# Kernel tuning notes

Hardware: AMD Instinct MI355X
Metric: run time of the kernel (lower is better)

Reference implementation:

```python
import jax, jax.numpy as jnp
import numpy as np

N_NODES = 100000
N_EDGES = 1600000
HID = 128
EDGE_DIM = 32
GN_EPS = 1e-5


def setup_inputs() -> dict:
    key = jax.random.key(0)
    ks = jax.random.split(key, 8)
    s = 0.05
    return {
        "x": jax.random.normal(ks[0], (N_NODES, HID), jnp.float32),
        "edge_index": jax.random.randint(ks[1], (2, N_EDGES), 0, N_NODES, jnp.int64),
        "edge_attr": jax.random.normal(ks[2], (N_EDGES, EDGE_DIM), jnp.float32),
        "edge_lin_W": jax.random.normal(ks[3], (EDGE_DIM, HID), jnp.float32) * s,
        "edge_lin_b": jnp.zeros((HID,), jnp.float32),
        "mlp_W1": jax.random.normal(ks[4], (HID, HID), jnp.float32) * s,
        "mlp_b1": jnp.zeros((HID,), jnp.float32),
        "mlp_W2": jax.random.normal(ks[5], (HID, HID), jnp.float32) * s,
        "mlp_b2": jnp.zeros((HID,), jnp.float32),
        "gn_weight": jnp.ones((HID,), jnp.float32),
        "gn_bias": jnp.zeros((HID,), jnp.float32),
        "gn_mean_scale": jnp.ones((HID,), jnp.float32),
    }


def reference(x, edge_index, edge_attr, edge_lin_W, edge_lin_b,
              mlp_W1, mlp_b1, mlp_W2, mlp_b2,
              gn_weight, gn_bias, gn_mean_scale):
    src, dst = edge_index[0], edge_index[1]
    # GINEConv message: ReLU(x_j + Lin(edge_attr)), sum-aggregated at dst
    e = edge_attr @ edge_lin_W + edge_lin_b            # [E, HID]
    msg = jax.nn.relu(x[src] + e)                      # [E, HID]
    agg = jax.ops.segment_sum(msg, dst, num_segments=x.shape[0])  # [N, HID]
    # update MLP on (1+eps)*x + agg, eps = 0
    h = agg + x
    h = jax.nn.relu(h @ mlp_W1 + mlp_b1) @ mlp_W2 + mlp_b2
    # GraphNorm with batch=None -> single graph: global node stats
    mean = jnp.mean(h, axis=0, keepdims=True)          # [1, HID]
    sub = h - gn_mean_scale * mean
    var = jnp.mean(sub * sub, axis=0, keepdims=True)
    out = gn_weight * sub / jnp.sqrt(var + GN_EPS) + gn_bias
    # final ReLU; dropout is identity at eval
    return jax.nn.relu(out)
```

## Files before the change

### kernel.cpp

```cpp
#include <hip/hip_runtime.h>
#include <stdint.h>

#define HID 128
#define EDIM 32

typedef __attribute__((ext_vector_type(8))) short bf16x8;
typedef __attribute__((ext_vector_type(4))) float f4_t;

static __device__ __forceinline__ unsigned short f2bf(float f) {
  union { float f; unsigned int u; } v; v.f = f;
  return (unsigned short)((v.u + 0x7fffu + ((v.u >> 16) & 1u)) >> 16);
}

static __device__ __forceinline__ float bf2f(short s) {
  union { unsigned int u; float f; } v;
  v.u = ((unsigned int)(unsigned short)s) << 16;
  return v.f;
}

static __device__ __forceinline__ void atomAddF(float* p, float v) {
#if defined(__gfx950__) || defined(__gfx942__) || defined(__gfx90a__)
  unsafeAtomicAdd(p, v);
#else
  atomicAdd(p, v);
#endif
}

__global__ __launch_bounds__(256) void hist_xperm(const int* __restrict__ ei,
                                                  const float* __restrict__ x,
                                                  unsigned int* __restrict__ counts,
                                                  unsigned short* __restrict__ xPerm,
                                                  int nE, int nNodes, int doPerm) {
  int tid = blockIdx.x * blockDim.x + threadIdx.x;
  const int stride = gridDim.x * blockDim.x;
  for (int i = tid; i < nE; i += stride) atomicAdd(&counts[ei[nE + i]], 1u);
  if (doPerm) {
    const int nCh = nNodes * 16;
    for (int j = tid; j < nCh; j += stride) {
      const int node = j >> 4, g = j & 15;
      const float* xp = x + (size_t)node * HID + g;
      bf16x8 o;
#pragma unroll
      for (int k = 0; k < 8; ++k) o[k] = (short)f2bf(xp[k * 16]);
      *(bf16x8*)(xPerm + (size_t)node * HID + g * 8) = o;
    }
  }
}

__global__ __launch_bounds__(1024) void chunk_sum(const unsigned int* __restrict__ counts,
                                                  unsigned int* __restrict__ chunkSum, int N) {
  __shared__ unsigned int wsum[16];
  const int tid = threadIdx.x;
  const int i = blockIdx.x * 1024 + tid;
  unsigned int v = (i < N) ? counts[i] : 0u;
#pragma unroll
  for (int d = 1; d < 64; d <<= 1) v += (unsigned int)__shfl_xor((int)v, d);
  if ((tid & 63) == 0) wsum[tid >> 6] = v;
  __syncthreads();
  if (tid < 16) {
    unsigned int t = wsum[tid];
#pragma unroll
    for (int d = 1; d < 16; d <<= 1) t += (unsigned int)__shfl_xor((int)t, d);
    if (tid == 0) chunkSum[blockIdx.x] = t;
  }
}

__global__ __launch_bounds__(256) void scan_chunks(const unsigned int* __restrict__ chunkSum,
                                                   unsigned int* __restrict__ chunkOff,
                                                   unsigned int* __restrict__ offsets,
                                                   int nChunks, int N) {
  __shared__ unsigned int wsum[4];
  const int tid = threadIdx.x, lane = tid & 63, w = tid >> 6;
  unsigned int v = (tid < nChunks) ? chunkSum[tid] : 0u;
  unsigned int s = v;
#pragma unroll
  for (int d = 1; d < 64; d <<= 1) {
    unsigned int t = (unsigned int)__shfl_up((int)s, d);
    if (lane >= d) s += t;
  }
  if (lane == 63) wsum[w] = s;
  __syncthreads();
  unsigned int wOff = 0;
  for (int k = 0; k < w; ++k) wOff += wsum[k];
  if (tid < nChunks) chunkOff[tid] = wOff + s - v;
  if (tid == nChunks - 1) offsets[N] = wOff + s;
}

__global__ __launch_bounds__(1024) void scan_local(const unsigned int* __restrict__ counts,
                                                   const unsigned int* __restrict__ chunkOff,
                                                   unsigned int* __restrict__ offsets,
                                                   unsigned int* __restrict__ cursors, int N) {
  __shared__ unsigned int wsum[16];
  const int tid = threadIdx.x, lane = tid & 63, w = tid >> 6;
  const int i = blockIdx.x * 1024 + tid;
  unsigned int v = (i < N) ? counts[i] : 0u;
  unsigned int s = v;
#pragma unroll
  for (int d = 1; d < 64; d <<= 1) {
    unsigned int t = (unsigned int)__shfl_up((int)s, d);
    if (lane >= d) s += t;
  }
  if (lane == 63) wsum[w] = s;
  __syncthreads();
  unsigned int wOff = 0;
  for (int k = 0; k < w; ++k) wOff += wsum[k];
  if (i < N) {
    const unsigned int ex = chunkOff[blockIdx.x] + wOff + (s - v);
    offsets[i] = ex;
    cursors[i] = ex;
  }
}

__global__ __launch_bounds__(256) void scatter_conv(const int* __restrict__ ei,
                                                    const float* __restrict__ ea,
                                                    unsigned int* __restrict__ cursors,
                                                    unsigned int* __restrict__ sortedSrc,
                                                    unsigned short* __restrict__ eaSorted,
                                                    int nE) {
  const int lane = threadIdx.x & 63;
  const int q = lane & 3;
  int t = blockIdx.x * blockDim.x + threadIdx.x;
  const int eStride = (gridDim.x * blockDim.x) >> 2;
  for (int e = t >> 2; e < nE; e += eStride) {
    unsigned int pos = 0;
    if (q == 0) {
      const int d = ei[nE + e];
      pos = atomicAdd(&cursors[d], 1u);
      sortedSrc[pos] = (unsigned int)ei[e];
    }
    pos = (unsigned int)__shfl((int)pos, lane & ~3);
    const f4_t* ap = (const f4_t*)(ea + (size_t)e * EDIM + q * 8);
    f4_t a0 = __builtin_nontemporal_load(ap);
    f4_t a1 = __builtin_nontemporal_load(ap + 1);
    bf16x8 o;
#pragma unroll
    for (int k = 0; k < 4; ++k) { o[k] = (short)f2bf(a0[k]); o[k + 4] = (short)f2bf(a1[k]); }
    *(bf16x8*)(eaSorted + (size_t)pos * EDIM + q * 8) = o;
  }
}

__global__ __launch_bounds__(256) void scatter_min(const int* __restrict__ ei,
                                                   unsigned int* __restrict__ cursors,
                                                   unsigned int* __restrict__ sortedEid,
                                                   unsigned int* __restrict__ sortedSrc,
                                                   int nE) {
  int i = blockIdx.x * blockDim.x + threadIdx.x;
  const int stride = gridDim.x * blockDim.x;
  for (; i < nE; i += stride) {
    const int d = ei[nE + i];
    const unsigned int pos = atomicAdd(&cursors[d], 1u);
    sortedEid[pos] = (unsigned int)i;
    sortedSrc[pos] = (unsigned int)ei[i];
  }
}

__global__ __launch_bounds__(256) void agg_pair(
    const float* __restrict__ x, const unsigned short* __restrict__ xPerm,
    const unsigned short* __restrict__ eaSorted, const unsigned int* __restrict__ sortedSrc,
    const float* __restrict__ W, const float* __restrict__ bias,
    const unsigned int* __restrict__ offsets, float* __restrict__ h,
    int nNodes, int nPairs) {
  const int lane = threadIdx.x & 63;
  const int l15 = lane & 15;
  const int lq  = lane >> 4;

  bf16x8 Wf[8];
  float bv[8];
#pragma unroll
  for (int nt = 0; nt < 8; ++nt) {
#pragma unroll
    for (int j = 0; j < 8; ++j)
      Wf[nt][j] = (short)f2bf(W[(8 * lq + j) * HID + 16 * nt + l15]);
    bv[nt] = bias[16 * nt + l15];
  }

  int waveId = blockIdx.x * 4 + ((int)threadIdx.x >> 6);
  const int nWaves = gridDim.x * 4;

  auto LOADT = [&](unsigned int b, unsigned int end, bf16x8& af, bf16x8* xg) {
    const unsigned int sA = b + (unsigned int)l15;
    if (sA < end)
      af = __builtin_nontemporal_load((const bf16x8*)(eaSorted + (size_t)sA * EDIM + lq * 8));
    else
      af = bf16x8{0, 0, 0, 0, 0, 0, 0, 0};
#pragma unroll
    for (int r = 0; r < 4; ++r) {
      unsigned int sl = b + (unsigned int)(lq * 4 + r);
      unsigned int cl = sl < end ? sl : end - 1;
      const unsigned int src = sortedSrc[cl];
      xg[r] = *(const bf16x8*)(xPerm + (size_t)src * HID + l15 * 8);
    }
  };

  for (int p = waveId; p < nPairs; p += nWaves) {
    const int nA = p * 2;
    const int nB = (nA + 1 < nNodes) ? nA + 1 : nA;
    unsigned int bA = offsets[nA];
    const unsigned int eA = offsets[nA + 1];
    unsigned int bB = offsets[nB];
    const unsigned int eB = offsets[nB + 1];

    float accA[8] = {0, 0, 0, 0, 0, 0, 0, 0};
    float accB[8] = {0, 0, 0, 0, 0, 0, 0, 0};

    while (bA < eA || bB < eB) {
      const bool mA = bA < eA, mB = bB < eB;
      bf16x8 afA, afB, xgA[4], xgB[4];
      if (mA) LOADT(bA, eA, afA, xgA);
      if (mB) LOADT(bB, eB, afB, xgB);

      if (mA) {
        f4_t acc[8];
#pragma unroll
        for (int nt = 0; nt < 8; ++nt) {
          f4_t c; c[0] = bv[nt]; c[1] = bv[nt]; c[2] = bv[nt]; c[3] = bv[nt];
          acc[nt] = __builtin_amdgcn_mfma_f32_16x16x32_bf16(afA, Wf[nt], c, 0, 0, 0);
        }
#pragma unroll
        for (int r = 0; r < 4; ++r) {
          if (bA + (unsigned int)(lq * 4 + r) < eA) {
#pragma unroll
            for (int nt = 0; nt < 8; ++nt)
              accA[nt] += fmaxf(acc[nt][r] + bf2f(xgA[r][nt]), 0.f);
          }
        }
        bA += 16;
      }

      if (mB) {
        f4_t acc[8];
#pragma unroll
        for (int nt = 0; nt < 8; ++nt) {
          f4_t c; c[0] = bv[nt]; c[1] = bv[nt]; c[2] = bv[nt]; c[3] = bv[nt];
          acc[nt] = __builtin_amdgcn_mfma_f32_16x16x32_bf16(afB, Wf[nt], c, 0, 0, 0);
        }
#pragma unroll
        for (int r = 0; r < 4; ++r) {
          if (bB + (unsigned int)(lq * 4 + r) < eB) {
#pragma unroll
            for (int nt = 0; nt < 8; ++nt)
              accB[nt] += fmaxf(acc[nt][r] + bf2f(xgB[r][nt]), 0.f);
          }
        }
        bB += 16;
      }
    }

#pragma unroll
    for (int nt = 0; nt < 8; ++nt) {
      accA[nt] += __shfl_xor(accA[nt], 16);
      accA[nt] += __shfl_xor(accA[nt], 32);
      accB[nt] += __shfl_xor(accB[nt], 16);
      accB[nt] += __shfl_xor(accB[nt], 32);
    }

    const int c0 = 32 * lq + l15;
    const size_t rowA = (size_t)nA * HID;
    const size_t rowB = (size_t)nB * HID;
    h[rowA + c0]      = accA[2 * lq]     + x[rowA + c0];
    h[rowA + c0 + 16] = accA[2 * lq + 1] + x[rowA + c0 + 16];
    h[rowB + c0]      = accB[2 * lq]     + x[rowB + c0];
    h[rowB + c0 + 16] = accB[2 * lq + 1] + x[rowB + c0 + 16];
  }
}

__global__ __launch_bounds__(256) void agg_fb(
    const float* __restrict__ x, const float* __restrict__ ea,
    const float* __restrict__ W, const float* __restrict__ bias,
    const unsigned int* __restrict__ offsets, const unsigned int* __restrict__ sortedEid,
    const unsigned int* __restrict__ sortedSrc, float* __restrict__ h, int nNodes) {
  const int lane = threadIdx.x & 63;
  const int l15 = lane & 15;
  const int lq  = lane >> 4;

  bf16x8 Wf[8];
  float bv[8];
#pragma unroll
  for (int nt = 0; nt < 8; ++nt) {
#pragma unroll
    for (int j = 0; j < 8; ++j)
      Wf[nt][j] = (short)f2bf(W[(8 * lq + j) * HID + 16 * nt + l15]);
    bv[nt] = bias[16 * nt + l15];
  }

  int waveId = blockIdx.x * 4 + ((int)threadIdx.x >> 6);
  const int nWaves = gridDim.x * 4;

  for (int n = waveId; n < nNodes; n += nWaves) {
    const unsigned int beg = offsets[n];
    const unsigned int end = offsets[n + 1];
    float accv[8] = {0, 0, 0, 0, 0, 0, 0, 0};

    for (unsigned int base = beg; base < end; base += 16) {
      bf16x8 af = {0, 0, 0, 0, 0, 0, 0, 0};
      const unsigned int slotA = base + (unsigned int)l15;
      if (slotA < end) {
        const unsigned int eidA = sortedEid[slotA];
        const float* ap = ea + (size_t)eidA * EDIM + 8 * lq;
        f4_t a0 = *(const f4_t*)ap;
        f4_t a1 = *(const f4_t*)(ap + 4);
#pragma unroll
        for (int j = 0; j < 4; ++j) { af[j] = (short)f2bf(a0[j]); af[j + 4] = (short)f2bf(a1[j]); }
      }
      f4_t acc[8];
#pragma unroll
      for (int nt = 0; nt < 8; ++nt) {
        f4_t c; c[0] = bv[nt]; c[1] = bv[nt]; c[2] = bv[nt]; c[3] = bv[nt];
        acc[nt] = __builtin_amdgcn_mfma_f32_16x16x32_bf16(af, Wf[nt], c, 0, 0, 0);
      }
#pragma unroll
      for (int r = 0; r < 4; ++r) {
        const unsigned int slot = base + (unsigned int)(lq * 4 + r);
        if (slot < end) {
          const int s = (int)sortedSrc[slot];
          const float* xp = x + (size_t)s * HID + l15;
#pragma unroll
          for (int nt = 0; nt < 8; ++nt)
            accv[nt] += fmaxf(acc[nt][r] + xp[nt * 16], 0.f);
        }
      }
    }

#pragma unroll
    for (int nt = 0; nt < 8; ++nt) {
      accv[nt] += __shfl_xor(accv[nt], 16);
      accv[nt] += __shfl_xor(accv[nt], 32);
    }
    const int c0 = 32 * lq + l15;
    const size_t rowOff = (size_t)n * HID;
    h[rowOff + c0]      = accv[2 * lq]     + x[rowOff + c0];
    h[rowOff + c0 + 16] = accv[2 * lq + 1] + x[rowOff + c0 + 16];
  }
}

__global__ __launch_bounds__(256) void node_kernel(
    float* __restrict__ h, const float* __restrict__ W1, const float* __restrict__ b1,
    const float* __restrict__ W2, const float* __restrict__ b2,
    float* __restrict__ stats, int nNodes, int nTiles) {
  __shared__ unsigned short sW1[128 * 128];
  __shared__ unsigned short sW2[128 * 128];
  __shared__ unsigned short sH1[4][16 * 128];

  for (int idx = threadIdx.x; idx < 128 * 128; idx += 256) {
    int n = idx & 127, k = idx >> 7;
    int off = n * 128 + ((((k >> 3) ^ (n & 15))) << 3) + (k & 7);
    sW1[off] = f2bf(W1[k * HID + n]);
    sW2[off] = f2bf(W2[k * HID + n]);
  }
  __syncthreads();

  const int lane = threadIdx.x & 63;
  const int l15 = lane & 15, lq = lane >> 4;
  const int wv = threadIdx.x >> 6;
  unsigned short* hb = &sH1[wv][0];

  float b1v[8], b2v[8];
#pragma unroll
  for (int nt = 0; nt < 8; ++nt) { b1v[nt] = b1[nt * 16 + l15]; b2v[nt] = b2[nt * 16 + l15]; }
  float ssum[8] = {0, 0, 0, 0, 0, 0, 0, 0};
  float ssq[8]  = {0, 0, 0, 0, 0, 0, 0, 0};

  int waveId = blockIdx.x * 4 + wv;
  const int nWaves = gridDim.x * 4;

  for (int tile = waveId; tile < nTiles; tile += nWaves) {
    const int r0 = tile << 4;
    int rr = r0 + l15; if (rr >= nNodes) rr = nNodes - 1;
    const float* hp = h + (size_t)rr * HID;

    bf16x8 af[4];
#pragma unroll
    for (int kt = 0; kt < 4; ++kt) {
      const int k0 = kt * 32 + 8 * lq;
      f4_t u0 = *(const f4_t*)(hp + k0);
      f4_t u1 = *(const f4_t*)(hp + k0 + 4);
#pragma unroll
      for (int j = 0; j < 4; ++j) {
        af[kt][j]     = (short)f2bf(u0[j]);
        af[kt][j + 4] = (short)f2bf(u1[j]);
      }
    }

    f4_t acc[8];
#pragma unroll
    for (int nt = 0; nt < 8; ++nt) {
      f4_t c; c[0] = b1v[nt]; c[1] = b1v[nt]; c[2] = b1v[nt]; c[3] = b1v[nt];
#pragma unroll
      for (int kt = 0; kt < 4; ++kt) {
        bf16x8 wf = *(const bf16x8*)&sW1[(nt * 16 + l15) * 128 + ((((kt * 4 + lq) ^ l15)) << 3)];
        c = __builtin_amdgcn_mfma_f32_16x16x32_bf16(af[kt], wf, c, 0, 0, 0);
      }
      acc[nt] = c;
    }

#pragma unroll
    for (int nt = 0; nt < 8; ++nt) {
      const int ghi = 2 * nt + (l15 >> 3);
#pragma unroll
      for (int r = 0; r < 4; ++r) {
        const int row = lq * 4 + r;
        hb[row * 128 + ((ghi ^ (row & 15)) << 3) + (l15 & 7)] = f2bf(fmaxf(acc[nt][r], 0.f));
      }
    }
    asm volatile("s_waitcnt lgkmcnt(0)" ::: "memory");
    __builtin_amdgcn_sched_barrier(0);

    bf16x8 af2[4];
#pragma unroll
    for (int kt = 0; kt < 4; ++kt)
      af2[kt] = *(const bf16x8*)&hb[l15 * 128 + ((((kt * 4 + lq) ^ l15)) << 3)];

    f4_t acc2[8];
#pragma unroll
    for (int nt = 0; nt < 8; ++nt) {
      f4_t c; c[0] = b2v[nt]; c[1] = b2v[nt]; c[2] = b2v[nt]; c[3] = b2v[nt];
#pragma unroll
      for (int kt = 0; kt < 4; ++kt) {
        bf16x8 wf = *(const bf16x8*)&sW2[(nt * 16 + l15) * 128 + ((((kt * 4 + lq) ^ l15)) << 3)];
        c = __builtin_amdgcn_mfma_f32_16x16x32_bf16(af2[kt], wf, c, 0, 0, 0);
      }
      acc2[nt] = c;
    }

#pragma unroll
    for (int nt = 0; nt < 8; ++nt) {
#pragma unroll
      for (int r = 0; r < 4; ++r) {
        const int row = r0 + lq * 4 + r;
        if (row < nNodes) {
          float v = acc2[nt][r];
          h[(size_t)row * HID + nt * 16 + l15] = v;
          ssum[nt] += v; ssq[nt] += v * v;
        }
      }
    }
  }

#pragma unroll
  for (int nt = 0; nt < 8; ++nt) {
    float a = ssum[nt], b = ssq[nt];
    a += __shfl_xor(a, 16); b += __shfl_xor(b, 16);
    a += __shfl_xor(a, 32); b += __shfl_xor(b, 32);
    if (lq == 0) {
      atomAddF(&stats[nt * 16 + l15], a);
      atomAddF(&stats[HID + nt * 16 + l15], b);
    }
  }
}

__global__ void norm_prep(float* __restrict__ stats, const float* __restrict__ gw,
                          const float* __restrict__ gb, const float* __restrict__ gs,
                          int nNodes) {
  int c = threadIdx.x;
  if (c < HID) {
    float invN = 1.f / (float)nNodes;
    float m   = stats[c] * invN;
    float msq = stats[HID + c] * invN;
    float s   = gs[c];
    float var = msq - (2.f * s - s * s) * m * m;
    float A = gw[c] * rsqrtf(var + 1e-5f);
    float B = gb[c] - A * s * m;
    stats[2 * HID + c] = A;
    stats[3 * HID + c] = B;
  }
}

__global__ __launch_bounds__(256) void norm_kernel(const float* __restrict__ stats,
                                                   float* __restrict__ out, int total4) {
  const f4_t* A4 = (const f4_t*)(stats + 2 * HID);
  const f4_t* B4 = (const f4_t*)(stats + 3 * HID);
  int i = blockIdx.x * blockDim.x + threadIdx.x;
  const int stride = gridDim.x * blockDim.x;
  for (; i < total4; i += stride) {
    const int cg = i & 31;
    f4_t h = ((const f4_t*)out)[i];
    f4_t a = A4[cg], b = B4[cg];
    f4_t o;
#pragma unroll
    for (int j = 0; j < 4; ++j) o[j] = fmaxf(fmaf(h[j], a[j], b[j]), 0.f);
    ((f4_t*)out)[i] = o;
  }
}

extern "C" void kernel_launch(void* const* d_in, const int* in_sizes, int n_in,
                              void* d_out, int out_size, void* d_ws, size_t ws_size,
                              hipStream_t stream) {
  const float* x  = (const float*)d_in[0];
  const int*   ei = (const int*)d_in[1];
  const float* ea = (const float*)d_in[2];
  const float* eW = (const float*)d_in[3];
  const float* eb = (const float*)d_in[4];
  const float* W1 = (const float*)d_in[5];
  const float* b1 = (const float*)d_in[6];
  const float* W2 = (const float*)d_in[7];
  const float* b2 = (const float*)d_in[8];
  const float* gw = (const float*)d_in[9];
  const float* gb = (const float*)d_in[10];
  const float* gs = (const float*)d_in[11];
  float* out = (float*)d_out;

  const int nNodes = in_sizes[0] / HID;
  const int nE     = in_sizes[1] / 2;

  char* w = (char*)d_ws;
  const size_t offStats   = 0;
  const size_t offCounts  = 2048;
  const size_t offCursors = offCounts  + (size_t)nNodes * 4;
  const size_t offOffsets = offCursors + (size_t)nNodes * 4;
  const size_t offChunk   = offOffsets + (((size_t)(nNodes + 1) * 4 + 63) & ~63ull);
  const size_t offSS      = (offChunk + 2048 + 63) & ~63ull;
  const size_t offEaS     = offSS + (size_t)nE * 4;
  const size_t offXP      = offEaS + (size_t)nE * EDIM * 2;
  const size_t needFlat   = offXP + (size_t)nNodes * HID * 2;

  float* stats            = (float*)(w + offStats);
  unsigned int* counts    = (unsigned int*)(w + offCounts);
  unsigned int* cursors   = (unsigned int*)(w + offCursors);
  unsigned int* offsets   = (unsigned int*)(w + offOffsets);
  unsigned int* chunkSum  = (unsigned int*)(w + offChunk);
  unsigned int* chunkOff  = (unsigned int*)(w + offChunk + 1024);
  unsigned int* sortedSrc = (unsigned int*)(w + offSS);
  unsigned int* sortedEid = (unsigned int*)(w + offEaS);
  unsigned short* eaSorted= (unsigned short*)(w + offEaS);
  unsigned short* xPerm   = (unsigned short*)(w + offXP);

  const int flatMode = (ws_size >= needFlat) ? 1 : 0;

  hipMemsetAsync(d_ws, 0, offCursors, stream);

  hist_xperm<<<2048, 256, 0, stream>>>(ei, x, counts, xPerm, nE, nNodes, flatMode);

  const int nChunks = (nNodes + 1023) / 1024;
  chunk_sum<<<nChunks, 1024, 0, stream>>>(counts, chunkSum, nNodes);
  scan_chunks<<<1, 256, 0, stream>>>(chunkSum, chunkOff, offsets, nChunks, nNodes);
  scan_local<<<nChunks, 1024, 0, stream>>>(counts, chunkOff, offsets, cursors, nNodes);

  if (flatMode) {
    scatter_conv<<<2048, 256, 0, stream>>>(ei, ea, cursors, sortedSrc, eaSorted, nE);
    const int nPairs = (nNodes + 1) / 2;
    const int blocks = (nPairs + 7) / 8;
    agg_pair<<<blocks, 256, 0, stream>>>(x, xPerm, eaSorted, sortedSrc, eW, eb,
                                         offsets, out, nNodes, nPairs);
  } else {
    scatter_min<<<1024, 256, 0, stream>>>(ei, cursors, sortedEid, sortedSrc, nE);
    agg_fb<<<8192, 256, 0, stream>>>(x, ea, eW, eb, offsets, sortedEid, sortedSrc, out, nNodes);
  }

  const int nTiles = (nNodes + 15) >> 4;
  node_kernel<<<512, 256, 0, stream>>>(out, W1, b1, W2, b2, stats, nNodes, nTiles);

  norm_prep<<<1, 128, 0, stream>>>(stats, gw, gb, gs, nNodes);
  norm_kernel<<<2048, 256, 0, stream>>>(stats, out, nNodes * (HID / 4));
}
```

Before: 419.6 us.

## Aggregate three nodes per wave, prefetch source indices, store h in bf16

The aggregation kernel now handles three destination nodes per wave instead of two, giving more independent gathers in flight. It preloads up to 128 source indices with one coalesced load and hands them out by wave shuffles instead of scalar reads. When workspace allows, the aggregated h is written as bf16 into a separate buffer, so node_kernel reads half the bytes and skips its conversion. The cost is more register pressure from three accumulator sets and a larger workspace requirement.

Measured after the change: 497.0 us. 18.5% more time.

```diff
diff --git a/kernel.cpp b/kernel.cpp
--- a/kernel.cpp
+++ b/kernel.cpp
@@ -154,12 +154,13 @@
   }
 }
 
-__global__ __launch_bounds__(256) void agg_pair(
+template <int BF16H>
+__global__ __launch_bounds__(256) void agg_tri(
     const float* __restrict__ x, const unsigned short* __restrict__ xPerm,
     const unsigned short* __restrict__ eaSorted, const unsigned int* __restrict__ sortedSrc,
     const float* __restrict__ W, const float* __restrict__ bias,
     const unsigned int* __restrict__ offsets, float* __restrict__ h,
-    int nNodes, int nPairs) {
+    unsigned short* __restrict__ hBf, int nNodes, int nGroups) {
   const int lane = threadIdx.x & 63;
   const int l15 = lane & 15;
   const int lq  = lane >> 4;
@@ -177,90 +178,116 @@
   int waveId = blockIdx.x * 4 + ((int)threadIdx.x >> 6);
   const int nWaves = gridDim.x * 4;
 
-  auto LOADT = [&](unsigned int b, unsigned int end, bf16x8& af, bf16x8* xg) {
-    const unsigned int sA = b + (unsigned int)l15;
-    if (sA < end)
-      af = __builtin_nontemporal_load((const bf16x8*)(eaSorted + (size_t)sA * EDIM + lq * 8));
-    else
-      af = bf16x8{0, 0, 0, 0, 0, 0, 0, 0};
-#pragma unroll
-    for (int r = 0; r < 4; ++r) {
-      unsigned int sl = b + (unsigned int)(lq * 4 + r);
-      unsigned int cl = sl < end ? sl : end - 1;
-      const unsigned int src = sortedSrc[cl];
-      xg[r] = *(const bf16x8*)(xPerm + (size_t)src * HID + l15 * 8);
-    }
-  };
-
-  for (int p = waveId; p < nPairs; p += nWaves) {
-    const int nA = p * 2;
-    const int nB = (nA + 1 < nNodes) ? nA + 1 : nA;
-    unsigned int bA = offsets[nA];
-    const unsigned int eA = offsets[nA + 1];
-    unsigned int bB = offsets[nB];
-    const unsigned int eB = offsets[nB + 1];
-
-    float accA[8] = {0, 0, 0, 0, 0, 0, 0, 0};
-    float accB[8] = {0, 0, 0, 0, 0, 0, 0, 0};
-
-    while (bA < eA || bB < eB) {
-      const bool mA = bA < eA, mB = bB < eB;
-      bf16x8 afA, afB, xgA[4], xgB[4];
-      if (mA) LOADT(bA, eA, afA, xgA);
-      if (mB) LOADT(bB, eB, afB, xgB);
-
-      if (mA) {
-        f4_t acc[8];
-#pragma unroll
-        for (int nt = 0; nt < 8; ++nt) {
-          f4_t c; c[0] = bv[nt]; c[1] = bv[nt]; c[2] = bv[nt]; c[3] = bv[nt];
-          acc[nt] = __builtin_amdgcn_mfma_f32_16x16x32_bf16(afA, Wf[nt], c, 0, 0, 0);
+  for (int g = waveId; g < nGroups; g += nWaves) {
+    const int n0 = g * 3;
+    unsigned int beg[3], end[3];
+#pragma unroll
+    for (int m = 0; m < 3; ++m) {
+      const int nm = n0 + m;
+      if (nm < nNodes) { beg[m] = offsets[nm]; end[m] = offsets[nm + 1]; }
+      else { beg[m] = 0; end[m] = 0; }
+    }
+    const unsigned int s0 = beg[0];
+    unsigned int endC = end[2] > end[1] ? end[2] : end[1];
+    endC = endC > end[0] ? endC : end[0];
+
+    unsigned int srcP0 = 0, srcP1 = 0;
+    if (endC > s0) {
+      const unsigned int last = endC - 1;
+      unsigned int i0 = s0 + (unsigned int)lane;
+      unsigned int i1 = i0 + 64;
+      srcP0 = __builtin_nontemporal_load(&sortedSrc[i0 < last ? i0 : last]);
+      srcP1 = __builtin_nontemporal_load(&sortedSrc[i1 < last ? i1 : last]);
+    }
+
+    auto GETSRC = [&](unsigned int slot) -> unsigned int {
+      const int idx = (int)(slot - s0);
+      const unsigned int v0 = (unsigned int)__shfl((int)srcP0, idx & 63);
+      const unsigned int v1 = (unsigned int)__shfl((int)srcP1, idx & 63);
+      unsigned int v = (idx < 64) ? v0 : v1;
+      if (idx >= 128) v = sortedSrc[slot];
+      return v;
+    };
+
+    auto LOADT = [&](unsigned int b, unsigned int e, bf16x8& af, bf16x8* xg) {
+      const unsigned int sA = b + (unsigned int)l15;
+      if (sA < e)
+        af = __builtin_nontemporal_load((const bf16x8*)(eaSorted + (size_t)sA * EDIM + lq * 8));
+      else
+        af = bf16x8{0, 0, 0, 0, 0, 0, 0, 0};
+#pragma unroll
+      for (int r = 0; r < 4; ++r) {
+        unsigned int sl = b + (unsigned int)(lq * 4 + r);
+        unsigned int cl = sl < e ? sl : e - 1;
+        const unsigned int src = GETSRC(cl);
+        xg[r] = *(const bf16x8*)(xPerm + (size_t)src * HID + l15 * 8);
+      }
+    };
+
+    float acc0[8] = {0, 0, 0, 0, 0, 0, 0, 0};
+    float acc1[8] = {0, 0, 0, 0, 0, 0, 0, 0};
+    float acc2[8] = {0, 0, 0, 0, 0, 0, 0, 0};
+    float* accs[3] = {acc0, acc1, acc2};
+    unsigned int cur[3] = {beg[0], beg[1], beg[2]};
+
+    while (cur[0] < end[0] || cur[1] < end[1] || cur[2] < end[2]) {
+      bool mm[3];
+      bf16x8 af[3], xg[3][4];
+#pragma unroll
+      for (int m = 0; m < 3; ++m) {
+        mm[m] = cur[m] < end[m];
+        if (mm[m]) LOADT(cur[m], end[m], af[m], xg[m]);
+      }
+#pragma unroll
+      for (int m = 0; m < 3; ++m) {
+        if (mm[m]) {
+          f4_t acc[8];
+#pragma unroll
+          for (int nt = 0; nt < 8; ++nt) {
+            f4_t c; c[0] = bv[nt]; c[1] = bv[nt]; c[2] = bv[nt]; c[3] = bv[nt];
+            acc[nt] = __builtin_amdgcn_mfma_f32_16x16x32_bf16(af[m], Wf[nt], c, 0, 0, 0);
+          }
+          float* av = accs[m];
+#pragma unroll
+          for (int r = 0; r < 4; ++r) {
+            if (cur[m] + (unsigned int)(lq * 4 + r) < end[m]) {
+#pragma unroll
+              for (int nt = 0; nt < 8; ++nt)
+                av[nt] += fmaxf(acc[nt][r] + bf2f(xg[m][r][nt]), 0.f);
+            }
+          }
+          cur[m] += 16;
         }
-#pragma unroll
-        for (int r = 0; r < 4; ++r) {
-          if (bA + (unsigned int)(lq * 4 + r) < eA) {
-#pragma unroll
-            for (int nt = 0; nt < 8; ++nt)
-              accA[nt] += fmaxf(acc[nt][r] + bf2f(xgA[r][nt]), 0.f);
-          }
+      }
+    }
+
+#pragma unroll
+    for (int m = 0; m < 3; ++m) {
+      float* av = accs[m];
+#pragma unroll
+      for (int nt = 0; nt < 8; ++nt) {
+        av[nt] += __shfl_xor(av[nt], 16);
+        av[nt] += __shfl_xor(av[nt], 32);
+      }
+    }
+
+    const int c0 = 32 * lq + l15;
+#pragma unroll
+    for (int m = 0; m < 3; ++m) {
+      const int nm = n0 + m;
+      if (nm < nNodes) {
+        const size_t row = (size_t)nm * HID;
+        const float v0 = accs[m][2 * lq]     + x[row + c0];
+        const float v1 = accs[m][2 * lq + 1] + x[row + c0 + 16];
+        if (BF16H) {
+          hBf[row + c0]      = f2bf(v0);
+          hBf[row + c0 + 16] = f2bf(v1);
+        } else {
+          h[row + c0]      = v0;
+          h[row + c0 + 16] = v1;
         }
-        bA += 16;
-      }
-
-      if (mB) {
-        f4_t acc[8];
-#pragma unroll
-        for (int nt = 0; nt < 8; ++nt) {
-          f4_t c; c[0] = bv[nt]; c[1] = bv[nt]; c[2] = bv[nt]; c[3] = bv[nt];
-          acc[nt] = __builtin_amdgcn_mfma_f32_16x16x32_bf16(afB, Wf[nt], c, 0, 0, 0);
-        }
-#pragma unroll
-        for (int r = 0; r < 4; ++r) {
-          if (bB + (unsigned int)(lq * 4 + r) < eB) {
-#pragma unroll
-            for (int nt = 0; nt < 8; ++nt)
-              accB[nt] += fmaxf(acc[nt][r] + bf2f(xgB[r][nt]), 0.f);
-          }
-        }
-        bB += 16;
-      }
-    }
-
-#pragma unroll
-    for (int nt = 0; nt < 8; ++nt) {
-      accA[nt] += __shfl_xor(accA[nt], 16);
-      accA[nt] += __shfl_xor(accA[nt], 32);
-      accB[nt] += __shfl_xor(accB[nt], 16);
-      accB[nt] += __shfl_xor(accB[nt], 32);
-    }
-
-    const int c0 = 32 * lq + l15;
-    const size_t rowA = (size_t)nA * HID;
-    const size_t rowB = (size_t)nB * HID;
-    h[rowA + c0]      = accA[2 * lq]     + x[rowA + c0];
-    h[rowA + c0 + 16] = accA[2 * lq + 1] + x[rowA + c0 + 16];
-    h[rowB + c0]      = accB[2 * lq]     + x[rowB + c0];
-    h[rowB + c0 + 16] = accB[2 * lq + 1] + x[rowB + c0 + 16];
+      }
+    }
   }
 }
 
@@ -333,10 +360,12 @@
   }
 }
 
+template <int BF16H>
 __global__ __launch_bounds__(256) void node_kernel(
-    float* __restrict__ h, const float* __restrict__ W1, const float* __restrict__ b1,
+    const float* __restrict__ hF, const unsigned short* __restrict__ hBf,
+    const float* __restrict__ W1, const float* __restrict__ b1,
     const float* __restrict__ W2, const float* __restrict__ b2,
-    float* __restrict__ stats, int nNodes, int nTiles) {
+    float* __restrict__ h2out, float* __restrict__ stats, int nNodes, int nTiles) {
   __shared__ unsigned short sW1[128 * 128];
   __shared__ unsigned short sW2[128 * 128];
   __shared__ unsigned short sH1[4][16 * 128];
@@ -366,18 +395,25 @@
   for (int tile = waveId; tile < nTiles; tile += nWaves) {
     const int r0 = tile << 4;
     int rr = r0 + l15; if (rr >= nNodes) rr = nNodes - 1;
-    const float* hp = h + (size_t)rr * HID;
 
     bf16x8 af[4];
-#pragma unroll
-    for (int kt = 0; kt < 4; ++kt) {
-      const int k0 = kt * 32 + 8 * lq;
-      f4_t u0 = *(const f4_t*)(hp + k0);
-      f4_t u1 = *(const f4_t*)(hp + k0 + 4);
-#pragma unroll
-      for (int j = 0; j < 4; ++j) {
-        af[kt][j]     = (short)f2bf(u0[j]);
-        af[kt][j + 4] = (short)f2bf(u1[j]);
+    if (BF16H) {
+      const unsigned short* hp = hBf + (size_t)rr * HID;
+#pragma unroll
+      for (int kt = 0; kt < 4; ++kt)
+        af[kt] = *(const bf16x8*)(hp + kt * 32 + 8 * lq);
+    } else {
+      const float* hp = hF + (size_t)rr * HID;
+#pragma unroll
+      for (int kt = 0; kt < 4; ++kt) {
+        const int k0 = kt * 32 + 8 * lq;
+        f4_t u0 = *(const f4_t*)(hp + k0);
+        f4_t u1 = *(const f4_t*)(hp + k0 + 4);
+#pragma unroll
+        for (int j = 0; j < 4; ++j) {
+          af[kt][j]     = (short)f2bf(u0[j]);
+          af[kt][j + 4] = (short)f2bf(u1[j]);
+        }
       }
     }
 
@@ -429,7 +465,7 @@
         const int row = r0 + lq * 4 + r;
         if (row < nNodes) {
           float v = acc2[nt][r];
-          h[(size_t)row * HID + nt * 16 + l15] = v;
+          h2out[(size_t)row * HID + nt * 16 + l15] = v;
           ssum[nt] += v; ssq[nt] += v * v;
         }
       }
@@ -512,6 +548,8 @@
   const size_t offEaS     = offSS + (size_t)nE * 4;
   const size_t offXP      = offEaS + (size_t)nE * EDIM * 2;
   const size_t needFlat   = offXP + (size_t)nNodes * HID * 2;
+  const size_t offHBf     = needFlat;
+  const size_t needBf     = offHBf + (size_t)nNodes * HID * 2;
 
   float* stats            = (float*)(w + offStats);
   unsigned int* counts    = (unsigned int*)(w + offCounts);
@@ -523,31 +561,42 @@
   unsigned int* sortedEid = (unsigned int*)(w + offEaS);
   unsigned short* eaSorted= (unsigned short*)(w + offEaS);
   unsigned short* xPerm   = (unsigned short*)(w + offXP);
-
-  const int flatMode = (ws_size >= needFlat) ? 1 : 0;
+  unsigned short* hBf     = (unsigned short*)(w + offHBf);
+
+  const int mode = (ws_size >= needBf) ? 2 : (ws_size >= needFlat ? 1 : 0);
 
   hipMemsetAsync(d_ws, 0, offCursors, stream);
 
-  hist_xperm<<<2048, 256, 0, stream>>>(ei, x, counts, xPerm, nE, nNodes, flatMode);
+  hist_xperm<<<2048, 256, 0, stream>>>(ei, x, counts, xPerm, nE, nNodes, mode >= 1);
 
   const int nChunks = (nNodes + 1023) / 1024;
   chunk_sum<<<nChunks, 1024, 0, stream>>>(counts, chunkSum, nNodes);
   scan_chunks<<<1, 256, 0, stream>>>(chunkSum, chunkOff, offsets, nChunks, nNodes);
   scan_local<<<nChunks, 1024, 0, stream>>>(counts, chunkOff, offsets, cursors, nNodes);
 
-  if (flatMode) {
+  const int nTiles = (nNodes + 15) >> 4;
+
+  if (mode >= 1) {
     scatter_conv<<<2048, 256, 0, stream>>>(ei, ea, cursors, sortedSrc, eaSorted, nE);
-    const int nPairs = (nNodes + 1) / 2;
-    const int blocks = (nPairs + 7) / 8;
-    agg_pair<<<blocks, 256, 0, stream>>>(x, xPerm, eaSorted, sortedSrc, eW, eb,
-                                         offsets, out, nNodes, nPairs);
+    const int nGroups = (nNodes + 2) / 3;
+    const int blocks = (nGroups + 7) / 8;
+    if (mode == 2) {
+      agg_tri<1><<<blocks, 256, 0, stream>>>(x, xPerm, eaSorted, sortedSrc, eW, eb,
+                                             offsets, out, hBf, nNodes, nGroups);
+      node_kernel<1><<<512, 256, 0, stream>>>(nullptr, hBf, W1, b1, W2, b2, out, stats,
+                                              nNodes, nTiles);
+    } else {
+      agg_tri<0><<<blocks, 256, 0, stream>>>(x, xPerm, eaSorted, sortedSrc, eW, eb,
+                                             offsets, out, hBf, nNodes, nGroups);
+      node_kernel<0><<<512, 256, 0, stream>>>(out, nullptr, W1, b1, W2, b2, out, stats,
+                                              nNodes, nTiles);
+    }
   } else {
     scatter_min<<<1024, 256, 0, stream>>>(ei, cursors, sortedEid, sortedSrc, nE);
     agg_fb<<<8192, 256, 0, stream>>>(x, ea, eW, eb, offsets, sortedEid, sortedSrc, out, nNodes);
-  }
-
-  const int nTiles = (nNodes + 15) >> 4;
-  node_kernel<<<512, 256, 0, stream>>>(out, W1, b1, W2, b2, stats, nNodes, nTiles);
+    node_kernel<0><<<512, 256, 0, stream>>>(out, nullptr, W1, b1, W2, b2, out, stats,
+                                            nNodes, nTiles);
+  }
 
   norm_prep<<<1, 128, 0, stream>>>(stats, gw, gb, gs, nNodes);
   norm_kernel<<<2048, 256, 0, stream>>>(stats, out, nNodes * (HID / 4));
```
